# Performance work log

Hardware: AMD Instinct MI355X
Metric: run time of the kernel (lower is better)

The kernel has to match this reference:

```python
import jax, jax.numpy as jnp
import numpy as np

B, N, D, H, NW = 16, 400, 256, 8, 4
DH = D // H
EPS_LN = 1e-5

def _layer_norm(x, g, b):
    m = jnp.mean(x, axis=-1, keepdims=True)
    v = jnp.mean((x - m) ** 2, axis=-1, keepdims=True)
    return (x - m) / jnp.sqrt(v + EPS_LN) * g + b

def setup_inputs() -> dict:
    key = jax.random.key(0)
    ks = jax.random.split(key, 10)
    p = lambda k, shape: (jax.random.normal(k, shape, jnp.float32) * 0.02)
    return {
        'x': jax.random.normal(ks[0], (B, N, D), jnp.float32),
        'attention_weights': jax.random.normal(ks[1], (B, NW, N, N), jnp.float32),
        'Wq': p(ks[2], (D, D)), 'bq': jnp.zeros((D,), jnp.float32),
        'Wk': p(ks[3], (D, D)), 'bk': jnp.zeros((D,), jnp.float32),
        'Wv': p(ks[4], (D, D)), 'bv': jnp.zeros((D,), jnp.float32),
        'Wo': p(ks[5], (D, D)), 'bo': jnp.zeros((D,), jnp.float32),
        'g1': jnp.ones((D,), jnp.float32), 'beta1': jnp.zeros((D,), jnp.float32),
        'W1': p(ks[6], (4 * D, D)), 'b1': jnp.zeros((4 * D,), jnp.float32),
        'W2': p(ks[7], (D, 4 * D)), 'b2': jnp.zeros((D,), jnp.float32),
        'g2': jnp.ones((D,), jnp.float32), 'beta2': jnp.zeros((D,), jnp.float32),
    }

def reference(x, attention_weights, Wq, bq, Wk, bk, Wv, bv, Wo, bo,
              g1, beta1, W1, b1, W2, b2, g2, beta2):
    b, n, d = x.shape
    # QKV projections, split heads: [B, H, N, DH]
    q = (x @ Wq.T + bq).reshape(b, n, H, DH).transpose(0, 2, 1, 3)
    k = (x @ Wk.T + bk).reshape(b, n, H, DH).transpose(0, 2, 1, 3)
    v = (x @ Wv.T + bv).reshape(b, n, H, DH).transpose(0, 2, 1, 3)
    qk = jnp.einsum('bhnd,bhmd->bhnm', q, k) / np.sqrt(DH)  # [B,H,N,N]
    # signed attention averaged over the NW per-sample weight matrices
    nw = attention_weights.shape[1]
    scores = jnp.zeros_like(qk)
    for i in range(nw):  # small fixed count, not a data dim
        w = attention_weights[:, i][:, None, :, :]  # [B,1,N,N]
        s = qk * w
        e = jnp.exp(jnp.abs(s))
        scores = scores + jnp.sign(s) * e / (jnp.sum(e, axis=-1, keepdims=True) + 1e-10)
    scores = scores / nw
    attn_out = jnp.einsum('bhnm,bhmd->bhnd', scores, v)
    attn_out = attn_out.transpose(0, 2, 1, 3).reshape(b, n, d)
    attn_out = attn_out @ Wo.T + bo
    h = _layer_norm(x + attn_out, g1, beta1)
    ffn = jax.nn.relu(h @ W1.T + b1) @ W2.T + b2
    y = _layer_norm(h + ffn, g2, beta2)
    return (y, scores)
```

## Files before the change

kernel.cpp:

```cpp
#include <hip/hip_runtime.h>
#include <hip/hip_fp16.h>

typedef unsigned int uint32;

#define B_ 16
#define N_ 400
#define D_ 256
#define H_ 8
#define DH_ 32
#define NW_ 4

#if __has_builtin(__builtin_amdgcn_exp2f)
#define EXP2(x) __builtin_amdgcn_exp2f(x)
#else
#define EXP2(x) exp2f(x)
#endif

#define QK_SCL 0.2550348f

using bf16x8 = __attribute__((ext_vector_type(8))) short;
using f16x8  = __attribute__((ext_vector_type(8))) _Float16;
using f32x4  = __attribute__((ext_vector_type(4))) float;

__device__ __forceinline__ ushort f2b(float f) {
  uint32 u = __float_as_uint(f);
  uint32 r = (u + 0x7fffu + ((u >> 16) & 1u)) >> 16;
  return (ushort)r;
}
__device__ __forceinline__ float b2f(ushort u) {
  return __uint_as_float(((uint32)u) << 16);
}

__global__ __launch_bounds__(256) void convert_kernel(
    const float* __restrict__ x,  const float* __restrict__ wq,
    const float* __restrict__ wk, const float* __restrict__ wv,
    const float* __restrict__ wo, const float* __restrict__ w1,
    const float* __restrict__ w2,
    ushort* __restrict__ xb,  ushort* __restrict__ wqb,
    ushort* __restrict__ wkb, ushort* __restrict__ wvb,
    ushort* __restrict__ wob, ushort* __restrict__ w1b,
    ushort* __restrict__ w2b) {
  int gid = blockIdx.x * 256 + threadIdx.x;
  const float* src; ushort* dst;
  if      (gid < 409600) { src = x;  dst = xb;  }
  else if ((gid -= 409600) < 16384) { src = wq; dst = wqb; }
  else if ((gid -= 16384) < 16384)  { src = wk; dst = wkb; }
  else if ((gid -= 16384) < 16384)  { src = wv; dst = wvb; }
  else if ((gid -= 16384) < 16384)  { src = wo; dst = wob; }
  else if ((gid -= 16384) < 65536)  { src = w1; dst = w1b; }
  else { gid -= 65536; src = w2; dst = w2b; }
  float4 f = ((const float4*)src)[gid];
  ushort4 u;
  u.x = f2b(f.x); u.y = f2b(f.y); u.z = f2b(f.z); u.w = f2b(f.w);
  *(ushort4*)&dst[(size_t)gid * 4] = u;
}

__global__ __launch_bounds__(256) void qkv_gemm(
    const ushort* __restrict__ xb, const ushort* __restrict__ wq,
    const ushort* __restrict__ wk, const ushort* __restrict__ wv,
    const float* __restrict__ bq, const float* __restrict__ bk,
    const float* __restrict__ bv,
    _Float16* __restrict__ qh, _Float16* __restrict__ kh,
    _Float16* __restrict__ vt) {
  __shared__ __align__(16) ushort As[2][64 * 40];
  __shared__ __align__(16) ushort Ws[2][64 * 40];
  int z = blockIdx.z;
  const ushort* W = (z == 0) ? wq : (z == 1) ? wk : wv;
  const float* bias = (z == 0) ? bq : (z == 1) ? bk : bv;

  int t = threadIdx.x;
  int l = t & 63, w = t >> 6;
  int n0 = blockIdx.x * 64, m0 = blockIdx.y * 64;
  int srow = t >> 2, sc = (t & 3) * 8;
  int lrow = l & 15, lk = (l >> 4) * 8;

  const uint4* ag = (const uint4*)&xb[(size_t)(m0 + srow) * 256 + sc];
  const uint4* wg = (const uint4*)&W[(size_t)(n0 + srow) * 256 + sc];
  uint4 ar = ag[0], wr = wg[0];

  f32x4 acc[4];
#pragma unroll
  for (int nt = 0; nt < 4; nt++) acc[nt] = {0.f, 0.f, 0.f, 0.f};

  for (int kk = 0; kk < 8; kk++) {
    int cur = kk & 1;
    *(uint4*)&As[cur][srow * 40 + sc] = ar;
    *(uint4*)&Ws[cur][srow * 40 + sc] = wr;
    if (kk + 1 < 8) { ar = ag[(kk + 1) * 4]; wr = wg[(kk + 1) * 4]; }
    __syncthreads();
    bf16x8 af = *(const bf16x8*)&As[cur][(16 * w + lrow) * 40 + lk];
#pragma unroll
    for (int nt = 0; nt < 4; nt++) {
      bf16x8 bf = *(const bf16x8*)&Ws[cur][(nt * 16 + lrow) * 40 + lk];
      acc[nt] = __builtin_amdgcn_mfma_f32_16x16x32_bf16(af, bf, acc[nt], 0, 0, 0);
    }
  }

  int mb = m0 + 16 * w + (l >> 4) * 4;
  int bb = mb / 400;
  int mi = mb - bb * 400;
#pragma unroll
  for (int nt = 0; nt < 4; nt++) {
    int n = n0 + nt * 16 + lrow;
    float bvv = bias[n];
    if (z < 2) {
      _Float16* out = z ? kh : qh;
      float scl = z ? 1.f : QK_SCL;
      int hh = n >> 5, dd = n & 31;
      _Float16* dst = out + (((size_t)(bb * 8 + hh)) * 400 + mi) * 32 + dd;
#pragma unroll
      for (int r = 0; r < 4; r++)
        dst[(size_t)r * 32] = (_Float16)((acc[nt][r] + bvv) * scl);
    } else {
      _Float16 h4[4];
#pragma unroll
      for (int r = 0; r < 4; r++) h4[r] = (_Float16)(acc[nt][r] + bvv);
      *(uint2*)&vt[((size_t)bb * 256 + n) * 400 + mi] = *(uint2*)h4;
    }
  }
}

#define SP 416

__global__ __launch_bounds__(256) void attn_kernel(
    const _Float16* __restrict__ qh, const _Float16* __restrict__ kh,
    const _Float16* __restrict__ vt, const float* __restrict__ aw,
    float* __restrict__ scores, ushort* __restrict__ attnb) {
  __shared__ __align__(16) char smem[16 * SP * 2 + 256];
  __half* S = (__half*)smem;
  float* zin = (float*)(smem + 16 * SP * 2);

  int id = blockIdx.x;
  int c = ((id >> 6) << 3) | (id & 7);
  int hh = (id >> 3) & 7;
  int b = c / 25;
  int n0 = (c - b * 25) * 16;

  int t = threadIdx.x;
  int w = t >> 6, l = t & 63;
  int lq = l >> 4, lr = l & 15;

  {
    const _Float16* qbase = qh + (((size_t)(b * 8 + hh)) * 400 + n0) * 32;
    const _Float16* kbase = kh + ((size_t)(b * 8 + hh)) * 400 * 32;
    f16x8 af = *(const f16x8*)(qbase + lr * 32 + lq * 8);
    for (int mt = w; mt < 25; mt += 4) {
      f16x8 bf = *(const f16x8*)(kbase + (size_t)(mt * 16 + lr) * 32 + lq * 8);
      f32x4 cc = {0.f, 0.f, 0.f, 0.f};
      cc = __builtin_amdgcn_mfma_f32_16x16x32_f16(af, bf, cc, 0, 0, 0);
#pragma unroll
      for (int r = 0; r < 4; r++)
        S[(lq * 4 + r) * SP + mt * 16 + lr] = __float2half(cc[r]);
    }
  }
  __syncthreads();

  {
    int r = t >> 2, p = t & 3;
    int i = r >> 4, n = r & 15;
    const float* wrow = aw + (((size_t)(b * 4 + i)) * 400 + n0 + n) * 400;
    const __half* srow = S + n * SP;
    float z = 0.f;
    for (int m = p * 4; m < 400; m += 16) {
      float4 wv = *(const float4*)(wrow + m);
      float2 f0 = __half22float2(*(const __half2*)(srow + m));
      float2 f1 = __half22float2(*(const __half2*)(srow + m + 2));
      z += EXP2(fabsf(f0.x * wv.x)) + EXP2(fabsf(f0.y * wv.y)) +
           EXP2(fabsf(f1.x * wv.z)) + EXP2(fabsf(f1.y * wv.w));
    }
    z += __shfl_xor(z, 1);
    z += __shfl_xor(z, 2);
    if (p == 0) zin[r] = 0.25f / (z + 1e-10f);
  }
  __syncthreads();

  {
    int n = t >> 4, p = t & 15;
    float zz[4] = {zin[n], zin[16 + n], zin[32 + n], zin[48 + n]};
    __half* srow = S + n * SP;
    const float* awn = aw + (((size_t)(b * 4)) * 400 + n0 + n) * 400;
    float* scout = scores + (((size_t)(b * 8 + hh)) * 400 + n0 + n) * 400;
    for (int m = p * 4; m < 448; m += 64) {
      if (m < 400) {
        float2 f0 = __half22float2(*(const __half2*)(srow + m));
        float2 f1 = __half22float2(*(const __half2*)(srow + m + 2));
        float q0 = f0.x, q1 = f0.y, q2 = f1.x, q3 = f1.y;
        float s0 = 0.f, s1 = 0.f, s2 = 0.f, s3 = 0.f;
#pragma unroll
        for (int i = 0; i < 4; i++) {
          float4 wv = *(const float4*)(awn + (size_t)i * 160000 + m);
          float t0 = q0 * wv.x; s0 += copysignf(EXP2(fabsf(t0)) * zz[i], t0);
          float t1 = q1 * wv.y; s1 += copysignf(EXP2(fabsf(t1)) * zz[i], t1);
          float t2 = q2 * wv.z; s2 += copysignf(EXP2(fabsf(t2)) * zz[i], t2);
          float t3 = q3 * wv.w; s3 += copysignf(EXP2(fabsf(t3)) * zz[i], t3);
        }
        float4 o = {s0, s1, s2, s3};
        *(float4*)(scout + m) = o;
        __half h4[4] = {__float2half(s0), __float2half(s1),
                        __float2half(s2), __float2half(s3)};
        *(uint2*)(srow + m) = *(uint2*)h4;
      } else if (m < 416) {
        uint2 zero = {0u, 0u};
        *(uint2*)(srow + m) = zero;
      }
    }
  }
  __syncthreads();

  const _Float16* vbase = vt + (((size_t)b) * 256 + hh * 32) * 400;
  f32x4 a0 = {0.f, 0.f, 0.f, 0.f}, a1 = {0.f, 0.f, 0.f, 0.f};
  const _Float16* Sh = (const _Float16*)S;
  for (int c2 = w; c2 < 13; c2 += 4) {
    f16x8 sf = *(const f16x8*)(Sh + lr * SP + c2 * 32 + lq * 8);
    f16x8 v0 = *(const f16x8*)(vbase + (size_t)lr * 400 + c2 * 32 + lq * 8);
    f16x8 v1 = *(const f16x8*)(vbase + (size_t)(16 + lr) * 400 + c2 * 32 + lq * 8);
    a0 = __builtin_amdgcn_mfma_f32_16x16x32_f16(sf, v0, a0, 0, 0, 0);
    a1 = __builtin_amdgcn_mfma_f32_16x16x32_f16(sf, v1, a1, 0, 0, 0);
  }
  __syncthreads();
  float* Of = (float*)smem;
#pragma unroll
  for (int r = 0; r < 4; r++) {
    Of[(w * 16 + lq * 4 + r) * 32 + lr] = a0[r];
    Of[(w * 16 + lq * 4 + r) * 32 + 16 + lr] = a1[r];
  }
  __syncthreads();
  for (int o = t; o < 512; o += 256) {
    int n = o >> 5, d = o & 31;
    float s = Of[n * 32 + d] + Of[512 + n * 32 + d] +
              Of[1024 + n * 32 + d] + Of[1536 + n * 32 + d];
    attnb[((size_t)(b * 400 + n0 + n)) * 256 + hh * 32 + d] = f2b(s);
  }
}

#define HP 272
#define RP 1040

__global__ __launch_bounds__(512, 2) void tail_kernel(
    const ushort* __restrict__ attnb, const ushort* __restrict__ wob,
    const float* __restrict__ bo, const float* __restrict__ x,
    const float* __restrict__ g1, const float* __restrict__ be1,
    const ushort* __restrict__ w1b, const float* __restrict__ b1,
    const ushort* __restrict__ w2b, const float* __restrict__ b2,
    const float* __restrict__ g2, const float* __restrict__ be2,
    float* __restrict__ yout) {
  __shared__ __align__(16) ushort bufA[16 * HP];
  __shared__ __align__(16) ushort relu[16 * RP];
  __shared__ float lnS[16 * 8], lnQ[16 * 8];

  int m0 = blockIdx.x * 16;
  int t = threadIdx.x, w = t >> 6, l = t & 63;
  int lr = l & 15, lq = l >> 4;
  int row4 = lq * 4;

  {
    int row = t >> 5, c = (t & 31) * 8;
    *(uint4*)&bufA[row * HP + c] =
        *(const uint4*)&attnb[(size_t)(m0 + row) * 256 + c];
  }
  __syncthreads();

  f32x4 acc[2];
  acc[0] = {0.f, 0.f, 0.f, 0.f}; acc[1] = {0.f, 0.f, 0.f, 0.f};
  for (int ks = 0; ks < 8; ks++) {
    bf16x8 af = *(const bf16x8*)&bufA[lr * HP + ks * 32 + lq * 8];
#pragma unroll
    for (int nt = 0; nt < 2; nt++) {
      bf16x8 bf = *(const bf16x8*)&wob[(size_t)(w * 32 + nt * 16 + lr) * 256 +
                                       ks * 32 + lq * 8];
      acc[nt] = __builtin_amdgcn_mfma_f32_16x16x32_bf16(af, bf, acc[nt], 0, 0, 0);
    }
  }
  float vals[2][4];
  float rs[4] = {0.f, 0.f, 0.f, 0.f}, rq[4] = {0.f, 0.f, 0.f, 0.f};
#pragma unroll
  for (int nt = 0; nt < 2; nt++) {
    int n = w * 32 + nt * 16 + lr;
    float bon = bo[n];
#pragma unroll
    for (int r = 0; r < 4; r++) {
      float v = acc[nt][r] + bon + x[(size_t)(m0 + row4 + r) * 256 + n];
      vals[nt][r] = v;
      rs[r] += v; rq[r] += v * v;
    }
  }
#pragma unroll
  for (int r = 0; r < 4; r++) {
#pragma unroll
    for (int o = 1; o < 16; o <<= 1) {
      rs[r] += __shfl_xor(rs[r], o);
      rq[r] += __shfl_xor(rq[r], o);
    }
  }
  if (lr == 0) {
#pragma unroll
    for (int r = 0; r < 4; r++) {
      lnS[(row4 + r) * 8 + w] = rs[r];
      lnQ[(row4 + r) * 8 + w] = rq[r];
    }
  }
  __syncthreads();
  {
    float mean[4], rsig[4];
#pragma unroll
    for (int r = 0; r < 4; r++) {
      int m = row4 + r;
      float s = 0.f, q = 0.f;
#pragma unroll
      for (int j = 0; j < 8; j++) { s += lnS[m * 8 + j]; q += lnQ[m * 8 + j]; }
      float mu = s * (1.f / 256.f);
      float va = q * (1.f / 256.f) - mu * mu;
      mean[r] = mu; rsig[r] = rsqrtf(va + 1e-5f);
    }
#pragma unroll
    for (int nt = 0; nt < 2; nt++) {
      int n = w * 32 + nt * 16 + lr;
      float g = g1[n], be = be1[n];
#pragma unroll
      for (int r = 0; r < 4; r++) {
        float h = (vals[nt][r] - mean[r]) * rsig[r] * g + be;
        bufA[(row4 + r) * HP + n] = f2b(h);
      }
    }
  }
  __syncthreads();

  {
    f32x4 a1[8];
#pragma unroll
    for (int nt = 0; nt < 8; nt++) a1[nt] = {0.f, 0.f, 0.f, 0.f};
    for (int ks = 0; ks < 8; ks++) {
      bf16x8 af = *(const bf16x8*)&bufA[lr * HP + ks * 32 + lq * 8];
#pragma unroll
      for (int nt = 0; nt < 8; nt++) {
        bf16x8 bf = *(const bf16x8*)&w1b[(size_t)(w * 128 + nt * 16 + lr) * 256 +
                                         ks * 32 + lq * 8];
        a1[nt] = __builtin_amdgcn_mfma_f32_16x16x32_bf16(af, bf, a1[nt], 0, 0, 0);
      }
    }
#pragma unroll
    for (int nt = 0; nt < 8; nt++) {
      int n = w * 128 + nt * 16 + lr;
      float bn = b1[n];
#pragma unroll
      for (int r = 0; r < 4; r++) {
        float v = fmaxf(a1[nt][r] + bn, 0.f);
        relu[(row4 + r) * RP + n] = f2b(v);
      }
    }
  }
  __syncthreads();

  f32x4 a2[2];
  a2[0] = {0.f, 0.f, 0.f, 0.f}; a2[1] = {0.f, 0.f, 0.f, 0.f};
  for (int ks = 0; ks < 32; ks++) {
    bf16x8 af = *(const bf16x8*)&relu[lr * RP + ks * 32 + lq * 8];
#pragma unroll
    for (int nt = 0; nt < 2; nt++) {
      bf16x8 bf = *(const bf16x8*)&w2b[(size_t)(w * 32 + nt * 16 + lr) * 1024 +
                                       ks * 32 + lq * 8];
      a2[nt] = __builtin_amdgcn_mfma_f32_16x16x32_bf16(af, bf, a2[nt], 0, 0, 0);
    }
  }
  float vals2[2][4];
  float rs2[4] = {0.f, 0.f, 0.f, 0.f}, rq2[4] = {0.f, 0.f, 0.f, 0.f};
#pragma unroll
  for (int nt = 0; nt < 2; nt++) {
    int n = w * 32 + nt * 16 + lr;
    float bn = b2[n];
#pragma unroll
    for (int r = 0; r < 4; r++) {
      float v = a2[nt][r] + bn + b2f(bufA[(row4 + r) * HP + n]);
      vals2[nt][r] = v;
      rs2[r] += v; rq2[r] += v * v;
    }
  }
#pragma unroll
  for (int r = 0; r < 4; r++) {
#pragma unroll
    for (int o = 1; o < 16; o <<= 1) {
      rs2[r] += __shfl_xor(rs2[r], o);
      rq2[r] += __shfl_xor(rq2[r], o);
    }
  }
  if (lr == 0) {
#pragma unroll
    for (int r = 0; r < 4; r++) {
      lnS[(row4 + r) * 8 + w] = rs2[r];
      lnQ[(row4 + r) * 8 + w] = rq2[r];
    }
  }
  __syncthreads();
  {
    float mean[4], rsig[4];
#pragma unroll
    for (int r = 0; r < 4; r++) {
      int m = row4 + r;
      float s = 0.f, q = 0.f;
#pragma unroll
      for (int j = 0; j < 8; j++) { s += lnS[m * 8 + j]; q += lnQ[m * 8 + j]; }
      float mu = s * (1.f / 256.f);
      float va = q * (1.f / 256.f) - mu * mu;
      mean[r] = mu; rsig[r] = rsqrtf(va + 1e-5f);
    }
#pragma unroll
    for (int nt = 0; nt < 2; nt++) {
      int n = w * 32 + nt * 16 + lr;
      float g = g2[n], be = be2[n];
#pragma unroll
      for (int r = 0; r < 4; r++) {
        float y = (vals2[nt][r] - mean[r]) * rsig[r] * g + be;
        yout[(size_t)(m0 + row4 + r) * 256 + n] = y;
      }
    }
  }
}

extern "C" void kernel_launch(void* const* d_in, const int* in_sizes, int n_in,
                              void* d_out, int out_size, void* d_ws,
                              size_t ws_size, hipStream_t stream) {
  const float* x   = (const float*)d_in[0];
  const float* aw  = (const float*)d_in[1];
  const float* Wq  = (const float*)d_in[2];
  const float* bq  = (const float*)d_in[3];
  const float* Wk  = (const float*)d_in[4];
  const float* bk  = (const float*)d_in[5];
  const float* Wv  = (const float*)d_in[6];
  const float* bv  = (const float*)d_in[7];
  const float* Wo  = (const float*)d_in[8];
  const float* bo  = (const float*)d_in[9];
  const float* g1  = (const float*)d_in[10];
  const float* be1 = (const float*)d_in[11];
  const float* W1  = (const float*)d_in[12];
  const float* b1  = (const float*)d_in[13];
  const float* W2  = (const float*)d_in[14];
  const float* b2  = (const float*)d_in[15];
  const float* g2  = (const float*)d_in[16];
  const float* be2 = (const float*)d_in[17];

  if (ws_size < 34340864) return;

  char* ws = (char*)d_ws;
  ushort*   xb    = (ushort*)(ws + 0);
  ushort*   wqb   = (ushort*)(ws + 3276800);
  ushort*   wkb   = (ushort*)(ws + 3407872);
  ushort*   wvb   = (ushort*)(ws + 3538944);
  ushort*   wob   = (ushort*)(ws + 3670016);
  ushort*   w1b   = (ushort*)(ws + 3801088);
  ushort*   w2b   = (ushort*)(ws + 4325376);
  _Float16* qhb   = (_Float16*)(ws + 4849664);
  _Float16* khb   = (_Float16*)(ws + 8126464);
  _Float16* vtb   = (_Float16*)(ws + 11403264);
  ushort*   attnb = (ushort*)(ws + 14680064);

  float* yout   = (float*)d_out;
  float* scores = yout + 1638400;

  convert_kernel<<<2368, 256, 0, stream>>>(x, Wq, Wk, Wv, Wo, W1, W2,
                                           xb, wqb, wkb, wvb, wob, w1b, w2b);
  qkv_gemm<<<dim3(4, 100, 3), 256, 0, stream>>>(
      xb, wqb, wkb, wvb, bq, bk, bv, qhb, khb, vtb);
  attn_kernel<<<3200, 256, 0, stream>>>(qhb, khb, vtb, aw, scores, attnb);
  tail_kernel<<<400, 512, 0, stream>>>(attnb, wob, bo, x, g1, be1,
                                       w1b, b1, w2b, b2, g2, be2, yout);
}
```

Before: 294.0 us.

## Read attention weights once, stage exp terms in LDS, retile tail kernel

The attention kernel now reads each attention-weight row once: it computes the exp terms, stores the signed values as bf16 in shared memory, and reuses them in the normalisation pass instead of re-reading global memory and recomputing exp. Scores are written with nontemporal stores. The tail kernel drops to 256 threads with four tiles per wave, and Wo/W1/W2 are pre-swizzled into a tile-contiguous layout during conversion to coalesce MFMA operand loads. In exchange, attention uses much more LDS (about 64KB), which may reduce occupancy, and the bf16 staging adds rounding error.

Result: slower. 354.8 us (+20.7%).

```diff
diff --git a/kernel.cpp b/kernel.cpp
--- a/kernel.cpp
+++ b/kernel.cpp
@@ -29,6 +29,14 @@
 }
 __device__ __forceinline__ float b2f(ushort u) {
   return __uint_as_float(((uint32)u) << 16);
+}
+__device__ __forceinline__ void unpack2(uint32 u, float* o) {
+  o[0] = __uint_as_float(u << 16);
+  o[1] = __uint_as_float(u & 0xffff0000u);
+}
+__device__ __forceinline__ uint32 packbf(float a, float b) {
+  return __builtin_amdgcn_perm(__float_as_uint(b), __float_as_uint(a),
+                               0x07060302u);
 }
 
 __global__ __launch_bounds__(256) void convert_kernel(
@@ -41,18 +49,29 @@
     ushort* __restrict__ wob, ushort* __restrict__ w1b,
     ushort* __restrict__ w2b) {
   int gid = blockIdx.x * 256 + threadIdx.x;
-  const float* src; ushort* dst;
-  if      (gid < 409600) { src = x;  dst = xb;  }
-  else if ((gid -= 409600) < 16384) { src = wq; dst = wqb; }
-  else if ((gid -= 16384) < 16384)  { src = wk; dst = wkb; }
-  else if ((gid -= 16384) < 16384)  { src = wv; dst = wvb; }
-  else if ((gid -= 16384) < 16384)  { src = wo; dst = wob; }
-  else if ((gid -= 16384) < 65536)  { src = w1; dst = w1b; }
-  else { gid -= 65536; src = w2; dst = w2b; }
+  const float* src; ushort* dst; int didx;
+  if (gid < 409600) { src = x; dst = xb; didx = gid * 4; }
+  else if ((gid -= 409600) < 16384) { src = wq; dst = wqb; didx = gid * 4; }
+  else if ((gid -= 16384) < 16384)  { src = wk; dst = wkb; didx = gid * 4; }
+  else if ((gid -= 16384) < 16384)  { src = wv; dst = wvb; didx = gid * 4; }
+  else if ((gid -= 16384) < 16384) {
+    int n = gid >> 6, kc = (gid & 63) * 4;
+    src = wo; dst = wob;
+    didx = (((n >> 4) * 8 + (kc >> 5)) << 9) + ((n & 15) << 5) + (kc & 31);
+  } else if ((gid -= 16384) < 65536) {
+    int n = gid >> 6, kc = (gid & 63) * 4;
+    src = w1; dst = w1b;
+    didx = (((n >> 4) * 8 + (kc >> 5)) << 9) + ((n & 15) << 5) + (kc & 31);
+  } else {
+    gid -= 65536;
+    int n = gid >> 8, kc = (gid & 255) * 4;
+    src = w2; dst = w2b;
+    didx = (((n >> 4) * 32 + (kc >> 5)) << 9) + ((n & 15) << 5) + (kc & 31);
+  }
   float4 f = ((const float4*)src)[gid];
   ushort4 u;
   u.x = f2b(f.x); u.y = f2b(f.y); u.z = f2b(f.z); u.w = f2b(f.w);
-  *(ushort4*)&dst[(size_t)gid * 4] = u;
+  *(ushort4*)&dst[didx] = u;
 }
 
 __global__ __launch_bounds__(256) void qkv_gemm(
@@ -120,15 +139,16 @@
   }
 }
 
-#define SP 416
+#define SPV 424
+#define STP 400
 
 __global__ __launch_bounds__(256) void attn_kernel(
     const _Float16* __restrict__ qh, const _Float16* __restrict__ kh,
     const _Float16* __restrict__ vt, const float* __restrict__ aw,
     float* __restrict__ scores, ushort* __restrict__ attnb) {
-  __shared__ __align__(16) char smem[16 * SP * 2 + 256];
-  __half* S = (__half*)smem;
-  float* zin = (float*)(smem + 16 * SP * 2);
+  __shared__ __align__(16) __half S[16 * SPV];
+  __shared__ __align__(16) ushort st[4][16 * STP];
+  __shared__ float zin[64];
 
   int id = blockIdx.x;
   int c = ((id >> 6) << 3) | (id & 7);
@@ -150,56 +170,77 @@
       cc = __builtin_amdgcn_mfma_f32_16x16x32_f16(af, bf, cc, 0, 0, 0);
 #pragma unroll
       for (int r = 0; r < 4; r++)
-        S[(lq * 4 + r) * SP + mt * 16 + lr] = __float2half(cc[r]);
-    }
-  }
-  __syncthreads();
-
-  {
-    int r = t >> 2, p = t & 3;
-    int i = r >> 4, n = r & 15;
-    const float* wrow = aw + (((size_t)(b * 4 + i)) * 400 + n0 + n) * 400;
-    const __half* srow = S + n * SP;
-    float z = 0.f;
-    for (int m = p * 4; m < 400; m += 16) {
-      float4 wv = *(const float4*)(wrow + m);
-      float2 f0 = __half22float2(*(const __half2*)(srow + m));
-      float2 f1 = __half22float2(*(const __half2*)(srow + m + 2));
-      z += EXP2(fabsf(f0.x * wv.x)) + EXP2(fabsf(f0.y * wv.y)) +
-           EXP2(fabsf(f1.x * wv.z)) + EXP2(fabsf(f1.y * wv.w));
-    }
-    z += __shfl_xor(z, 1);
-    z += __shfl_xor(z, 2);
-    if (p == 0) zin[r] = 0.25f / (z + 1e-10f);
+        S[(lq * 4 + r) * SPV + mt * 16 + lr] = __float2half(cc[r]);
+    }
   }
   __syncthreads();
 
   {
     int n = t >> 4, p = t & 15;
-    float zz[4] = {zin[n], zin[16 + n], zin[32 + n], zin[48 + n]};
-    __half* srow = S + n * SP;
-    const float* awn = aw + (((size_t)(b * 4)) * 400 + n0 + n) * 400;
+    const __half* srow = S + n * SPV;
+#pragma unroll
+    for (int i = 0; i < 4; i++) {
+      const float* wrow = aw + (((size_t)(b * 4 + i)) * 400 + n0 + n) * 400;
+      ushort* srt = &st[i][n * STP];
+      float z = 0.f;
+      for (int m = p * 4; m < 400; m += 64) {
+        float4 wv = *(const float4*)(wrow + m);
+        uint2 sv = *(const uint2*)(srow + m);
+        float2 f0 = __half22float2(*(const __half2*)&sv.x);
+        float2 f1 = __half22float2(*(const __half2*)&sv.y);
+        float t0 = f0.x * wv.x, t1 = f0.y * wv.y;
+        float t2 = f1.x * wv.z, t3 = f1.y * wv.w;
+        float e0 = EXP2(fabsf(t0)), e1 = EXP2(fabsf(t1));
+        float e2 = EXP2(fabsf(t2)), e3 = EXP2(fabsf(t3));
+        z += (e0 + e1) + (e2 + e3);
+        uint2 pk;
+        pk.x = packbf(copysignf(e0, t0), copysignf(e1, t1));
+        pk.y = packbf(copysignf(e2, t2), copysignf(e3, t3));
+        *(uint2*)(srt + m) = pk;
+      }
+      z += __shfl_xor(z, 1);
+      z += __shfl_xor(z, 2);
+      z += __shfl_xor(z, 4);
+      z += __shfl_xor(z, 8);
+      if (p == 0) zin[i * 16 + n] = 0.25f / (z + 1e-10f);
+    }
+  }
+  __syncthreads();
+
+  {
+    int n = t >> 4, p = t & 15;
+    float z0 = zin[n], z1 = zin[16 + n], z2 = zin[32 + n], z3 = zin[48 + n];
+    __half* srow = S + n * SPV;
+    const ushort* s0 = &st[0][n * STP];
+    const ushort* s1 = &st[1][n * STP];
+    const ushort* s2 = &st[2][n * STP];
+    const ushort* s3 = &st[3][n * STP];
     float* scout = scores + (((size_t)(b * 8 + hh)) * 400 + n0 + n) * 400;
-    for (int m = p * 4; m < 448; m += 64) {
+    for (int m = p * 4; m < 424; m += 64) {
       if (m < 400) {
-        float2 f0 = __half22float2(*(const __half2*)(srow + m));
-        float2 f1 = __half22float2(*(const __half2*)(srow + m + 2));
-        float q0 = f0.x, q1 = f0.y, q2 = f1.x, q3 = f1.y;
-        float s0 = 0.f, s1 = 0.f, s2 = 0.f, s3 = 0.f;
-#pragma unroll
-        for (int i = 0; i < 4; i++) {
-          float4 wv = *(const float4*)(awn + (size_t)i * 160000 + m);
-          float t0 = q0 * wv.x; s0 += copysignf(EXP2(fabsf(t0)) * zz[i], t0);
-          float t1 = q1 * wv.y; s1 += copysignf(EXP2(fabsf(t1)) * zz[i], t1);
-          float t2 = q2 * wv.z; s2 += copysignf(EXP2(fabsf(t2)) * zz[i], t2);
-          float t3 = q3 * wv.w; s3 += copysignf(EXP2(fabsf(t3)) * zz[i], t3);
+        uint2 a0 = *(const uint2*)(s0 + m);
+        uint2 a1 = *(const uint2*)(s1 + m);
+        uint2 a2 = *(const uint2*)(s2 + m);
+        uint2 a3 = *(const uint2*)(s3 + m);
+        float v0[4], v1[4], v2[4], v3[4];
+        unpack2(a0.x, &v0[0]); unpack2(a0.y, &v0[2]);
+        unpack2(a1.x, &v1[0]); unpack2(a1.y, &v1[2]);
+        unpack2(a2.x, &v2[0]); unpack2(a2.y, &v2[2]);
+        unpack2(a3.x, &v3[0]); unpack2(a3.y, &v3[2]);
+        f32x4 o;
+#pragma unroll
+        for (int j = 0; j < 4; j++) {
+          float s = v0[j] * z0;
+          s = fmaf(v1[j], z1, s);
+          s = fmaf(v2[j], z2, s);
+          s = fmaf(v3[j], z3, s);
+          o[j] = s;
         }
-        float4 o = {s0, s1, s2, s3};
-        *(float4*)(scout + m) = o;
-        __half h4[4] = {__float2half(s0), __float2half(s1),
-                        __float2half(s2), __float2half(s3)};
+        __builtin_nontemporal_store(o, (f32x4*)(scout + m));
+        __half h4[4] = {__float2half(o[0]), __float2half(o[1]),
+                        __float2half(o[2]), __float2half(o[3])};
         *(uint2*)(srow + m) = *(uint2*)h4;
-      } else if (m < 416) {
+      } else {
         uint2 zero = {0u, 0u};
         *(uint2*)(srow + m) = zero;
       }
@@ -211,14 +252,14 @@
   f32x4 a0 = {0.f, 0.f, 0.f, 0.f}, a1 = {0.f, 0.f, 0.f, 0.f};
   const _Float16* Sh = (const _Float16*)S;
   for (int c2 = w; c2 < 13; c2 += 4) {
-    f16x8 sf = *(const f16x8*)(Sh + lr * SP + c2 * 32 + lq * 8);
+    f16x8 sf = *(const f16x8*)(Sh + lr * SPV + c2 * 32 + lq * 8);
     f16x8 v0 = *(const f16x8*)(vbase + (size_t)lr * 400 + c2 * 32 + lq * 8);
     f16x8 v1 = *(const f16x8*)(vbase + (size_t)(16 + lr) * 400 + c2 * 32 + lq * 8);
     a0 = __builtin_amdgcn_mfma_f32_16x16x32_f16(sf, v0, a0, 0, 0, 0);
     a1 = __builtin_amdgcn_mfma_f32_16x16x32_f16(sf, v1, a1, 0, 0, 0);
   }
   __syncthreads();
-  float* Of = (float*)smem;
+  float* Of = (float*)st;
 #pragma unroll
   for (int r = 0; r < 4; r++) {
     Of[(w * 16 + lq * 4 + r) * 32 + lr] = a0[r];
@@ -233,10 +274,10 @@
   }
 }
 
-#define HP 272
-#define RP 1040
-
-__global__ __launch_bounds__(512, 2) void tail_kernel(
+#define HP 280
+#define RP 1048
+
+__global__ __launch_bounds__(256) void tail_kernel(
     const ushort* __restrict__ attnb, const ushort* __restrict__ wob,
     const float* __restrict__ bo, const float* __restrict__ x,
     const float* __restrict__ g1, const float* __restrict__ be1,
@@ -246,36 +287,38 @@
     float* __restrict__ yout) {
   __shared__ __align__(16) ushort bufA[16 * HP];
   __shared__ __align__(16) ushort relu[16 * RP];
-  __shared__ float lnS[16 * 8], lnQ[16 * 8];
+  __shared__ float lnS[64], lnQ[64];
 
   int m0 = blockIdx.x * 16;
   int t = threadIdx.x, w = t >> 6, l = t & 63;
-  int lr = l & 15, lq = l >> 4;
-  int row4 = lq * 4;
-
-  {
-    int row = t >> 5, c = (t & 31) * 8;
-    *(uint4*)&bufA[row * HP + c] =
-        *(const uint4*)&attnb[(size_t)(m0 + row) * 256 + c];
-  }
-  __syncthreads();
-
-  f32x4 acc[2];
-  acc[0] = {0.f, 0.f, 0.f, 0.f}; acc[1] = {0.f, 0.f, 0.f, 0.f};
+  int lr = l & 15, lq = l >> 4, row4 = lq * 4;
+
+  {
+    int row = t >> 4, c0 = (t & 15) * 16;
+    *(uint4*)&bufA[row * HP + c0] =
+        *(const uint4*)&attnb[(size_t)(m0 + row) * 256 + c0];
+    *(uint4*)&bufA[row * HP + c0 + 8] =
+        *(const uint4*)&attnb[(size_t)(m0 + row) * 256 + c0 + 8];
+  }
+  __syncthreads();
+
+  f32x4 acc[4];
+#pragma unroll
+  for (int nt = 0; nt < 4; nt++) acc[nt] = {0.f, 0.f, 0.f, 0.f};
   for (int ks = 0; ks < 8; ks++) {
     bf16x8 af = *(const bf16x8*)&bufA[lr * HP + ks * 32 + lq * 8];
 #pragma unroll
-    for (int nt = 0; nt < 2; nt++) {
-      bf16x8 bf = *(const bf16x8*)&wob[(size_t)(w * 32 + nt * 16 + lr) * 256 +
-                                       ks * 32 + lq * 8];
+    for (int nt = 0; nt < 4; nt++) {
+      int tile = w * 4 + nt;
+      bf16x8 bf = *(const bf16x8*)&wob[((tile * 8 + ks) << 9) + lr * 32 + lq * 8];
       acc[nt] = __builtin_amdgcn_mfma_f32_16x16x32_bf16(af, bf, acc[nt], 0, 0, 0);
     }
   }
-  float vals[2][4];
+  float vals[4][4];
   float rs[4] = {0.f, 0.f, 0.f, 0.f}, rq[4] = {0.f, 0.f, 0.f, 0.f};
 #pragma unroll
-  for (int nt = 0; nt < 2; nt++) {
-    int n = w * 32 + nt * 16 + lr;
+  for (int nt = 0; nt < 4; nt++) {
+    int n = (w * 4 + nt) * 16 + lr;
     float bon = bo[n];
 #pragma unroll
     for (int r = 0; r < 4; r++) {
@@ -295,8 +338,8 @@
   if (lr == 0) {
 #pragma unroll
     for (int r = 0; r < 4; r++) {
-      lnS[(row4 + r) * 8 + w] = rs[r];
-      lnQ[(row4 + r) * 8 + w] = rq[r];
+      lnS[(row4 + r) * 4 + w] = rs[r];
+      lnQ[(row4 + r) * 4 + w] = rq[r];
     }
   }
   __syncthreads();
@@ -305,16 +348,15 @@
 #pragma unroll
     for (int r = 0; r < 4; r++) {
       int m = row4 + r;
-      float s = 0.f, q = 0.f;
-#pragma unroll
-      for (int j = 0; j < 8; j++) { s += lnS[m * 8 + j]; q += lnQ[m * 8 + j]; }
+      float s = lnS[m * 4] + lnS[m * 4 + 1] + lnS[m * 4 + 2] + lnS[m * 4 + 3];
+      float q = lnQ[m * 4] + lnQ[m * 4 + 1] + lnQ[m * 4 + 2] + lnQ[m * 4 + 3];
       float mu = s * (1.f / 256.f);
       float va = q * (1.f / 256.f) - mu * mu;
       mean[r] = mu; rsig[r] = rsqrtf(va + 1e-5f);
     }
 #pragma unroll
-    for (int nt = 0; nt < 2; nt++) {
-      int n = w * 32 + nt * 16 + lr;
+    for (int nt = 0; nt < 4; nt++) {
+      int n = (w * 4 + nt) * 16 + lr;
       float g = g1[n], be = be1[n];
 #pragma unroll
       for (int r = 0; r < 4; r++) {
@@ -326,21 +368,21 @@
   __syncthreads();
 
   {
-    f32x4 a1[8];
-#pragma unroll
-    for (int nt = 0; nt < 8; nt++) a1[nt] = {0.f, 0.f, 0.f, 0.f};
+    f32x4 a1[16];
+#pragma unroll
+    for (int nt = 0; nt < 16; nt++) a1[nt] = {0.f, 0.f, 0.f, 0.f};
     for (int ks = 0; ks < 8; ks++) {
       bf16x8 af = *(const bf16x8*)&bufA[lr * HP + ks * 32 + lq * 8];
 #pragma unroll
-      for (int nt = 0; nt < 8; nt++) {
-        bf16x8 bf = *(const bf16x8*)&w1b[(size_t)(w * 128 + nt * 16 + lr) * 256 +
-                                         ks * 32 + lq * 8];
+      for (int nt = 0; nt < 16; nt++) {
+        int tile = w * 16 + nt;
+        bf16x8 bf = *(const bf16x8*)&w1b[((tile * 8 + ks) << 9) + lr * 32 + lq * 8];
         a1[nt] = __builtin_amdgcn_mfma_f32_16x16x32_bf16(af, bf, a1[nt], 0, 0, 0);
       }
     }
 #pragma unroll
-    for (int nt = 0; nt < 8; nt++) {
-      int n = w * 128 + nt * 16 + lr;
+    for (int nt = 0; nt < 16; nt++) {
+      int n = (w * 16 + nt) * 16 + lr;
       float bn = b1[n];
 #pragma unroll
       for (int r = 0; r < 4; r++) {
@@ -351,22 +393,23 @@
   }
   __syncthreads();
 
-  f32x4 a2[2];
-  a2[0] = {0.f, 0.f, 0.f, 0.f}; a2[1] = {0.f, 0.f, 0.f, 0.f};
+  f32x4 a2[4];
+#pragma unroll
+  for (int nt = 0; nt < 4; nt++) a2[nt] = {0.f, 0.f, 0.f, 0.f};
   for (int ks = 0; ks < 32; ks++) {
     bf16x8 af = *(const bf16x8*)&relu[lr * RP + ks * 32 + lq * 8];
 #pragma unroll
-    for (int nt = 0; nt < 2; nt++) {
-      bf16x8 bf = *(const bf16x8*)&w2b[(size_t)(w * 32 + nt * 16 + lr) * 1024 +
-                                       ks * 32 + lq * 8];
+    for (int nt = 0; nt < 4; nt++) {
+      int tile = w * 4 + nt;
+      bf16x8 bf = *(const bf16x8*)&w2b[((tile * 32 + ks) << 9) + lr * 32 + lq * 8];
       a2[nt] = __builtin_amdgcn_mfma_f32_16x16x32_bf16(af, bf, a2[nt], 0, 0, 0);
     }
   }
-  float vals2[2][4];
+  float vals2[4][4];
   float rs2[4] = {0.f, 0.f, 0.f, 0.f}, rq2[4] = {0.f, 0.f, 0.f, 0.f};
 #pragma unroll
-  for (int nt = 0; nt < 2; nt++) {
-    int n = w * 32 + nt * 16 + lr;
+  for (int nt = 0; nt < 4; nt++) {
+    int n = (w * 4 + nt) * 16 + lr;
     float bn = b2[n];
 #pragma unroll
     for (int r = 0; r < 4; r++) {
@@ -383,11 +426,12 @@
       rq2[r] += __shfl_xor(rq2[r], o);
     }
   }
+  __syncthreads();
   if (lr == 0) {
 #pragma unroll
     for (int r = 0; r < 4; r++) {
-      lnS[(row4 + r) * 8 + w] = rs2[r];
-      lnQ[(row4 + r) * 8 + w] = rq2[r];
+      lnS[(row4 + r) * 4 + w] = rs2[r];
+      lnQ[(row4 + r) * 4 + w] = rq2[r];
     }
   }
   __syncthreads();
@@ -396,16 +440,15 @@
 #pragma unroll
     for (int r = 0; r < 4; r++) {
       int m = row4 + r;
-      float s = 0.f, q = 0.f;
-#pragma unroll
-      for (int j = 0; j < 8; j++) { s += lnS[m * 8 + j]; q += lnQ[m * 8 + j]; }
+      float s = lnS[m * 4] + lnS[m * 4 + 1] + lnS[m * 4 + 2] + lnS[m * 4 + 3];
+      float q = lnQ[m * 4] + lnQ[m * 4 + 1] + lnQ[m * 4 + 2] + lnQ[m * 4 + 3];
       float mu = s * (1.f / 256.f);
       float va = q * (1.f / 256.f) - mu * mu;
       mean[r] = mu; rsig[r] = rsqrtf(va + 1e-5f);
     }
 #pragma unroll
-    for (int nt = 0; nt < 2; nt++) {
-      int n = w * 32 + nt * 16 + lr;
+    for (int nt = 0; nt < 4; nt++) {
+      int n = (w * 4 + nt) * 16 + lr;
       float g = g2[n], be = be2[n];
 #pragma unroll
       for (int r = 0; r < 4; r++) {
@@ -461,6 +504,6 @@
   qkv_gemm<<<dim3(4, 100, 3), 256, 0, stream>>>(
       xb, wqb, wkb, wvb, bq, bk, bv, qhb, khb, vtb);
   attn_kernel<<<3200, 256, 0, stream>>>(qhb, khb, vtb, aw, scores, attnb);
-  tail_kernel<<<400, 512, 0, stream>>>(attnb, wob, bo, x, g1, be1,
+  tail_kernel<<<400, 256, 0, stream>>>(attnb, wob, bo, x, g1, be1,
                                        w1b, b1, w2b, b2, g2, be2, yout);
 }
```
